# Performance work log

Measured on AMD Instinct MI355X. Metric: run time of the kernel, lower is better.

The kernel has to match this reference:

```python
import jax, jax.numpy as jnp
import numpy as np

V, D, H, L, E = 50000, 512, 512, 4, 40000


def setup_inputs() -> dict:
    key = jax.random.key(0)
    k1, k2, k3 = jax.random.split(key, 3)
    node_embeddings = jax.random.normal(k1, (V, D), dtype=jnp.float32)
    adjacency = jax.random.randint(k2, (L, E, 2), 0, V, dtype=jnp.int32)
    W = jax.random.normal(k3, (L, D, H), dtype=jnp.float32) * (1.0 / np.sqrt(D))
    return {"node_embeddings": node_embeddings, "adjacency": adjacency, "W": W}


def reference(node_embeddings, adjacency, W):
    # adjacency: [L, E, 2] with [:, :, 0] = source node, [:, :, 1] = target node
    src = adjacency[..., 0]  # [L, E]
    tgt = adjacency[..., 1]  # [L, E]
    # Gather source states per edge and apply per-edge-type linear message fn.
    # edge_source_states: [L, E, D]; messages: [L, E, H]
    messages = jnp.einsum("led,ldh->leh", node_embeddings[src], W)
    # Scatter-aggregate (sum) all messages to their target nodes.
    num_nodes = node_embeddings.shape[0]
    aggregated = jax.ops.segment_sum(
        messages.reshape(-1, messages.shape[-1]),  # [L*E, H]
        tgt.reshape(-1),
        num_segments=num_nodes,
    )  # [V, H]
    # message_activation_before_aggregation = False -> activation after aggregation
    return jax.nn.relu(aggregated)
```

## Files before the change

kernel.cpp:

```cpp
#include <hip/hip_runtime.h>
#include <hip/hip_bf16.h>

#define NV 50000
#define VP2 50176
#define ND 512
#define NH 512
#define NL 4
#define NE 40000
#define CAP 16
#define KTOT 2048
#define NKT 32
#define NWG2 392

typedef short bf16x8 __attribute__((ext_vector_type(8)));
typedef float f32x4  __attribute__((ext_vector_type(4)));

__device__ __forceinline__ unsigned short f2bf(float f) {
    unsigned int u = __float_as_uint(f);
    u += 0x7FFFu + ((u >> 16) & 1u);
    return (unsigned short)(u >> 16);
}
__device__ __forceinline__ unsigned pack_bf2(float x, float y) {
    return (unsigned)f2bf(x) | ((unsigned)f2bf(y) << 16);
}

#define GLL16(gp, lp) __builtin_amdgcn_global_load_lds( \
    (const __attribute__((address_space(1))) void*)(gp), \
    (__attribute__((address_space(3))) void*)(lp), 16, 0, 0)

__global__ void wt2_kernel(const float* __restrict__ W, unsigned short* __restrict__ Wt2) {
    int idx = blockIdx.x * 256 + threadIdx.x;
    int l = idx >> 18;
    int r = idx & 262143;
    int k = r >> 9;
    int h = r & 511;
    Wt2[((size_t)h << 11) + (l << 9) + k] = f2bf(W[idx]);
}

__global__ void place_kernel(const int* __restrict__ adj, int* __restrict__ cnt,
                             int* __restrict__ list) {
    int i = blockIdx.x * 256 + threadIdx.x;
    int2 p = ((const int2*)adj)[i];
    int l = i / NE;
    int cell = p.y * NL + l;
    int pos = atomicAdd(&cnt[cell], 1);
    if (pos < CAP) list[cell * CAP + pos] = p.x;
}

__global__ void __launch_bounds__(256)
agg_pull(const float* __restrict__ emb, const int* __restrict__ cnt,
         const int* __restrict__ list, unsigned* __restrict__ agg2) {
    const int wid  = blockIdx.x * 4 + (threadIdx.x >> 6);
    const int lane = threadIdx.x & 63;
    const int t    = wid >> 2;
    const int l    = wid & 3;
    const int cell = wid;
    const size_t dst = (size_t)t * 1024 + l * 256 + lane;

    int n = cnt[cell]; if (n > CAP) n = CAP;
    const int* lst = list + cell * CAP;

    float2 s0 = {0.f,0.f}, s1 = {0.f,0.f}, s2 = {0.f,0.f}, s3 = {0.f,0.f};
    int j = 0;
    for (; j + 2 <= n; j += 2) {
        const float2* p0 = (const float2*)(emb + (size_t)lst[j]     * ND) + lane;
        const float2* p1 = (const float2*)(emb + (size_t)lst[j + 1] * ND) + lane;
        float2 a0 = p0[0], a1 = p0[64], a2 = p0[128], a3 = p0[192];
        float2 b0 = p1[0], b1 = p1[64], b2 = p1[128], b3 = p1[192];
        s0.x += a0.x + b0.x; s0.y += a0.y + b0.y;
        s1.x += a1.x + b1.x; s1.y += a1.y + b1.y;
        s2.x += a2.x + b2.x; s2.y += a2.y + b2.y;
        s3.x += a3.x + b3.x; s3.y += a3.y + b3.y;
    }
    if (j < n) {
        const float2* p0 = (const float2*)(emb + (size_t)lst[j] * ND) + lane;
        float2 a0 = p0[0], a1 = p0[64], a2 = p0[128], a3 = p0[192];
        s0.x += a0.x; s0.y += a0.y;  s1.x += a1.x; s1.y += a1.y;
        s2.x += a2.x; s2.y += a2.y;  s3.x += a3.x; s3.y += a3.y;
    }
    agg2[dst]       = pack_bf2(s0.x, s0.y);
    agg2[dst + 64]  = pack_bf2(s1.x, s1.y);
    agg2[dst + 128] = pack_bf2(s2.x, s2.y);
    agg2[dst + 192] = pack_bf2(s3.x, s3.y);
}

__device__ __forceinline__ void stage_ht(
    int s, int t0, int n0, int wave, int lane,
    const unsigned short* __restrict__ agg2, const unsigned short* __restrict__ Wt2,
    unsigned short* sa0, unsigned short* sa1,
    unsigned short* sb0, unsigned short* sb1) {
    const int tile  = s >> 2, part = s & 3;
    const int lr8   = (part & 1) << 7;
    const int rowin = lane >> 3;
    const int slt   = (lane & 7) ^ rowin;
    const bool isA  = part < 2;
    const unsigned short* gsrc = isA ? agg2 : Wt2;
    const int gr0 = isA ? t0 : n0;
    unsigned short* ldsbase = isA ? ((tile & 1) ? sa1 : sa0)
                                  : ((tile & 1) ? sb1 : sb0);
#pragma unroll
    for (int c = 0; c < 2; ++c) {
        const int lr = lr8 + (wave * 2 + c) * 8;
        const unsigned short* src = gsrc
            + (size_t)(gr0 + lr + rowin) * KTOT + tile * 64 + slt * 8;
        GLL16(src, ldsbase + lr * 64);
    }
}

template<bool STG>
__device__ __forceinline__ void tile_step(
    int kt, int t0, int n0, int wave, int lane, int wm, int wn,
    const unsigned short* __restrict__ agg2, const unsigned short* __restrict__ Wt2,
    unsigned short* sa0, unsigned short* sa1,
    unsigned short* sb0, unsigned short* sb1,
    f32x4 (&acc)[8][4]) {
    const int laneL = lane & 15, laneH = lane >> 4;
    const int ax = laneL & 7;
    const unsigned short* pa = (kt & 1) ? sa1 : sa0;
    const unsigned short* pb = (kt & 1) ? sb1 : sb0;

    if (STG) {
        const int s1 = (kt + 1) * 4;
        stage_ht(s1 + 0, t0, n0, wave, lane, agg2, Wt2, sa0, sa1, sb0, sb1);
        stage_ht(s1 + 1, t0, n0, wave, lane, agg2, Wt2, sa0, sa1, sb0, sb1);
        stage_ht(s1 + 2, t0, n0, wave, lane, agg2, Wt2, sa0, sa1, sb0, sb1);
        stage_ht(s1 + 3, t0, n0, wave, lane, agg2, Wt2, sa0, sa1, sb0, sb1);
    }

    bf16x8 aF[4][2], bF[4][2];
#pragma unroll
    for (int ni = 0; ni < 4; ++ni)
#pragma unroll
        for (int ks = 0; ks < 2; ++ks) {
            const int row = wn * 64 + ni * 16 + laneL;
            bF[ni][ks] = *(const bf16x8*)(pb + row * 64 + (((ks * 4 + laneH) ^ ax) << 3));
        }
#pragma unroll
    for (int mi = 0; mi < 4; ++mi)
#pragma unroll
        for (int ks = 0; ks < 2; ++ks) {
            const int row = wm * 128 + mi * 16 + laneL;
            aF[mi][ks] = *(const bf16x8*)(pa + row * 64 + (((ks * 4 + laneH) ^ ax) << 3));
        }
#pragma unroll
    for (int mi = 0; mi < 4; ++mi)
#pragma unroll
        for (int ni = 0; ni < 4; ++ni)
#pragma unroll
            for (int ks = 0; ks < 2; ++ks)
                acc[mi][ni] = __builtin_amdgcn_mfma_f32_16x16x32_bf16(aF[mi][ks], bF[ni][ks], acc[mi][ni], 0, 0, 0);
#pragma unroll
    for (int mi = 0; mi < 4; ++mi)
#pragma unroll
        for (int ks = 0; ks < 2; ++ks) {
            const int row = wm * 128 + (mi + 4) * 16 + laneL;
            aF[mi][ks] = *(const bf16x8*)(pa + row * 64 + (((ks * 4 + laneH) ^ ax) << 3));
        }
#pragma unroll
    for (int mi = 0; mi < 4; ++mi)
#pragma unroll
        for (int ni = 0; ni < 4; ++ni)
#pragma unroll
            for (int ks = 0; ks < 2; ++ks)
                acc[mi + 4][ni] = __builtin_amdgcn_mfma_f32_16x16x32_bf16(aF[mi][ks], bF[ni][ks], acc[mi + 4][ni], 0, 0, 0);

    __syncthreads();
}

__global__ void __launch_bounds__(512)
gemm2p(const unsigned short* __restrict__ agg2,
       const unsigned short* __restrict__ Wt2,
       float* __restrict__ out) {
    __shared__ unsigned short s_a[2][256 * 64];
    __shared__ unsigned short s_b[2][256 * 64];

    const int orig = blockIdx.x;
    const int wgid = (orig & 7) * (NWG2 / 8) + (orig >> 3);
    const int mt = wgid >> 1, nt = wgid & 1;
    const int t0 = mt * 256, n0 = nt * 256;

    const int tid  = threadIdx.x;
    const int lane = tid & 63;
    const int wave = tid >> 6;
    const int wm   = wave >> 2;
    const int wn   = wave & 3;
    const int laneL = lane & 15, laneH = lane >> 4;

    f32x4 acc[8][4];
#pragma unroll
    for (int mi = 0; mi < 8; ++mi)
#pragma unroll
        for (int ni = 0; ni < 4; ++ni)
            acc[mi][ni] = (f32x4){0.f, 0.f, 0.f, 0.f};

    unsigned short* sa0 = &s_a[0][0]; unsigned short* sa1 = &s_a[1][0];
    unsigned short* sb0 = &s_b[0][0]; unsigned short* sb1 = &s_b[1][0];

#pragma unroll
    for (int p = 0; p < 4; ++p)
        stage_ht(p, t0, n0, wave, lane, agg2, Wt2, sa0, sa1, sb0, sb1);
    __syncthreads();

    for (int kt = 0; kt < NKT - 1; ++kt)
        tile_step<true>(kt, t0, n0, wave, lane, wm, wn, agg2, Wt2, sa0, sa1, sb0, sb1, acc);
    tile_step<false>(NKT - 1, t0, n0, wave, lane, wm, wn, agg2, Wt2, sa0, sa1, sb0, sb1, acc);

#pragma unroll
    for (int mi = 0; mi < 8; ++mi) {
#pragma unroll
        for (int i = 0; i < 4; ++i) {
            int t = t0 + wm * 128 + mi * 16 + laneH * 4 + i;
            if (t < NV) {
#pragma unroll
                for (int ni = 0; ni < 4; ++ni) {
                    int h = n0 + wn * 64 + ni * 16 + laneL;
                    out[(size_t)t * NH + h] = fmaxf(acc[mi][ni][i], 0.f);
                }
            }
        }
    }
}

__global__ void wt_legacy(const float* __restrict__ W, unsigned short* __restrict__ Wt) {
    int idx = blockIdx.x * 256 + threadIdx.x;
    int l = idx >> 18;
    int r = idx & 262143;
    int k = r >> 9;
    int h = r & 511;
    Wt[(l << 18) + (h << 9) + k] = f2bf(W[idx]);
}
__global__ void __launch_bounds__(256)
legacy_msg(const float* __restrict__ emb, const int* __restrict__ adj,
           const unsigned short* __restrict__ Wt, float* __restrict__ out) {
    __shared__ bf16x8 s_a[32 * 64];
    __shared__ int s_src[32];
    __shared__ int s_tgt[32];
    const int bx = blockIdx.x;
    const int l = bx / (NE / 32);
    const int ebase = (bx % (NE / 32)) * 32;
    const int tid = threadIdx.x, lane = tid & 63, wave = tid >> 6;
    if (tid < 32) {
        int2 p = *(const int2*)(adj + ((size_t)l * NE + ebase + tid) * 2);
        s_src[tid] = p.x; s_tgt[tid] = p.y;
    }
    __syncthreads();
    {
        const int r = tid >> 3, part = tid & 7, k0 = part * 64, rxx = r & 7;
        const float* g = emb + (size_t)s_src[r] * ND + k0;
#pragma unroll
        for (int j = 0; j < 8; ++j) {
            float4 f0 = *(const float4*)(g + j * 8);
            float4 f1 = *(const float4*)(g + j * 8 + 4);
            bf16x8 v;
            v[0]=(short)f2bf(f0.x); v[1]=(short)f2bf(f0.y);
            v[2]=(short)f2bf(f0.z); v[3]=(short)f2bf(f0.w);
            v[4]=(short)f2bf(f1.x); v[5]=(short)f2bf(f1.y);
            v[6]=(short)f2bf(f1.z); v[7]=(short)f2bf(f1.w);
            int slot = (k0 >> 3) + j;
            s_a[r * 64 + (slot ^ rxx)] = v;
        }
    }
    __syncthreads();
    const int c0 = wave * 128, laneL = lane & 15, laneH = lane >> 4, arx = laneL & 7;
    f32x4 acc[2][8];
#pragma unroll
    for (int mf = 0; mf < 2; ++mf)
#pragma unroll
        for (int nf = 0; nf < 8; ++nf) acc[mf][nf] = (f32x4){0.f,0.f,0.f,0.f};
    const bf16x8* wb = (const bf16x8*)(Wt + ((size_t)l << 18));
#pragma unroll
    for (int kc = 0; kc < 16; ++kc) {
        int slot = kc * 4 + laneH;
        bf16x8 a0 = s_a[laneL * 64 + (slot ^ arx)];
        bf16x8 a1 = s_a[(16 + laneL) * 64 + (slot ^ arx)];
#pragma unroll
        for (int nf = 0; nf < 8; ++nf) {
            bf16x8 b = wb[(c0 + nf * 16 + laneL) * 64 + slot];
            acc[0][nf] = __builtin_amdgcn_mfma_f32_16x16x32_bf16(a0, b, acc[0][nf], 0, 0, 0);
            acc[1][nf] = __builtin_amdgcn_mfma_f32_16x16x32_bf16(a1, b, acc[1][nf], 0, 0, 0);
        }
    }
#pragma unroll
    for (int mf = 0; mf < 2; ++mf)
#pragma unroll
        for (int nf = 0; nf < 8; ++nf) {
            int h = c0 + nf * 16 + laneL;
#pragma unroll
            for (int i = 0; i < 4; ++i) {
                int er = mf * 16 + laneH * 4 + i;
                atomicAdd(out + (size_t)s_tgt[er] * NH + h, acc[mf][nf][i]);
            }
        }
}
__global__ void legacy_relu(float* __restrict__ o, int n4) {
    int stride = gridDim.x * blockDim.x;
    for (int i = blockIdx.x * blockDim.x + threadIdx.x; i < n4; i += stride) {
        float4 v = ((float4*)o)[i];
        v.x = fmaxf(v.x, 0.f); v.y = fmaxf(v.y, 0.f);
        v.z = fmaxf(v.z, 0.f); v.w = fmaxf(v.w, 0.f);
        ((float4*)o)[i] = v;
    }
}

extern "C" void kernel_launch(void* const* d_in, const int* in_sizes, int n_in,
                              void* d_out, int out_size, void* d_ws, size_t ws_size,
                              hipStream_t stream) {
    const float* emb = (const float*)d_in[0];
    const int*   adj = (const int*)d_in[1];
    const float* W   = (const float*)d_in[2];
    float* out = (float*)d_out;
    char* ws = (char*)d_ws;

    unsigned short* Wt2  = (unsigned short*)ws;
    int*            cnt  = (int*)(ws + 2621440);
    int*            list = (int*)(ws + 3670016);
    unsigned short* agg2 = (unsigned short*)(ws + (16u << 20));

    const size_t need = (16u << 20) + (size_t)VP2 * KTOT * 2;

    if (ws_size >= need) {
        hipMemsetAsync(cnt, 0, (size_t)VP2 * NL * sizeof(int), stream);
        wt2_kernel<<<(NL * ND * NH) / 256, 256, 0, stream>>>(W, Wt2);
        place_kernel<<<(NL * NE) / 256, 256, 0, stream>>>(adj, cnt, list);
        agg_pull<<<(VP2 * NL) / 4, 256, 0, stream>>>(emb, cnt, list, (unsigned*)agg2);
        gemm2p<<<NWG2, 512, 0, stream>>>(agg2, Wt2, out);
    } else {
        hipMemsetAsync(d_out, 0, (size_t)out_size * sizeof(float), stream);
        wt_legacy<<<(NL * ND * NH) / 256, 256, 0, stream>>>(W, Wt2);
        legacy_msg<<<NL * (NE / 32), 256, 0, stream>>>(emb, adj, Wt2, out);
        legacy_relu<<<2048, 256, 0, stream>>>(out, out_size / 4);
    }
}
```

Baseline: 261.2 us.

## Load GEMM B fragments directly from global memory instead of staging through LDS

The GEMM kernel no longer stages the weight tile into shared memory. Each wave reads its B fragments straight from global memory (expected to hit in L2), and only the A tile is double-buffered in LDS. This halves LDS usage and the async copy traffic per tile, which could allow more workgroups per CU. The cost is exposed global-load latency on the B operand inside the MFMA loop, with no prefetch ahead of use.

```diff
diff --git a/kernel.cpp b/kernel.cpp
--- a/kernel.cpp
+++ b/kernel.cpp
@@ -84,26 +84,21 @@
     agg2[dst + 192] = pack_bf2(s3.x, s3.y);
 }
 
-__device__ __forceinline__ void stage_ht(
-    int s, int t0, int n0, int wave, int lane,
-    const unsigned short* __restrict__ agg2, const unsigned short* __restrict__ Wt2,
-    unsigned short* sa0, unsigned short* sa1,
-    unsigned short* sb0, unsigned short* sb1) {
-    const int tile  = s >> 2, part = s & 3;
-    const int lr8   = (part & 1) << 7;
+__device__ __forceinline__ void stage_a(
+    int kt, int t0, int wave, int lane,
+    const unsigned short* __restrict__ agg2,
+    unsigned short* sa0, unsigned short* sa1) {
     const int rowin = lane >> 3;
-    const int slt   = (lane & 7) ^ rowin;
-    const bool isA  = part < 2;
-    const unsigned short* gsrc = isA ? agg2 : Wt2;
-    const int gr0 = isA ? t0 : n0;
-    unsigned short* ldsbase = isA ? ((tile & 1) ? sa1 : sa0)
-                                  : ((tile & 1) ? sb1 : sb0);
-#pragma unroll
-    for (int c = 0; c < 2; ++c) {
-        const int lr = lr8 + (wave * 2 + c) * 8;
-        const unsigned short* src = gsrc
-            + (size_t)(gr0 + lr + rowin) * KTOT + tile * 64 + slt * 8;
-        GLL16(src, ldsbase + lr * 64);
+    const int slt   = lane & 7;
+    unsigned short* sa = (kt & 1) ? sa1 : sa0;
+    const int ko = kt * 64;
+#pragma unroll
+    for (int r = 0; r < 4; ++r) {
+        const int rb  = r * 64 + wave * 8;
+        const int row = rb + rowin;
+        const unsigned short* src = agg2
+            + (size_t)(t0 + row) * KTOT + ko + ((slt ^ (row & 7)) << 3);
+        GLL16(src, sa + rb * 64);
     }
 }
 
@@ -112,29 +107,24 @@
     int kt, int t0, int n0, int wave, int lane, int wm, int wn,
     const unsigned short* __restrict__ agg2, const unsigned short* __restrict__ Wt2,
     unsigned short* sa0, unsigned short* sa1,
-    unsigned short* sb0, unsigned short* sb1,
     f32x4 (&acc)[8][4]) {
     const int laneL = lane & 15, laneH = lane >> 4;
     const int ax = laneL & 7;
     const unsigned short* pa = (kt & 1) ? sa1 : sa0;
-    const unsigned short* pb = (kt & 1) ? sb1 : sb0;
-
-    if (STG) {
-        const int s1 = (kt + 1) * 4;
-        stage_ht(s1 + 0, t0, n0, wave, lane, agg2, Wt2, sa0, sa1, sb0, sb1);
-        stage_ht(s1 + 1, t0, n0, wave, lane, agg2, Wt2, sa0, sa1, sb0, sb1);
-        stage_ht(s1 + 2, t0, n0, wave, lane, agg2, Wt2, sa0, sa1, sb0, sb1);
-        stage_ht(s1 + 3, t0, n0, wave, lane, agg2, Wt2, sa0, sa1, sb0, sb1);
-    }
-
-    bf16x8 aF[4][2], bF[4][2];
+    const int ko = kt * 64;
+
+    if (STG) stage_a(kt + 1, t0, wave, lane, agg2, sa0, sa1);
+
+    bf16x8 bF[4][2];
 #pragma unroll
     for (int ni = 0; ni < 4; ++ni)
 #pragma unroll
         for (int ks = 0; ks < 2; ++ks) {
-            const int row = wn * 64 + ni * 16 + laneL;
-            bF[ni][ks] = *(const bf16x8*)(pb + row * 64 + (((ks * 4 + laneH) ^ ax) << 3));
-        }
+            const int h = n0 + wn * 64 + ni * 16 + laneL;
+            bF[ni][ks] = *(const bf16x8*)(Wt2 + (size_t)h * KTOT + ko + ks * 32 + laneH * 8);
+        }
+
+    bf16x8 aF[4][2];
 #pragma unroll
     for (int mi = 0; mi < 4; ++mi)
 #pragma unroll
@@ -168,11 +158,10 @@
 }
 
 __global__ void __launch_bounds__(512)
-gemm2p(const unsigned short* __restrict__ agg2,
-       const unsigned short* __restrict__ Wt2,
-       float* __restrict__ out) {
+gemm_bg(const unsigned short* __restrict__ agg2,
+        const unsigned short* __restrict__ Wt2,
+        float* __restrict__ out) {
     __shared__ unsigned short s_a[2][256 * 64];
-    __shared__ unsigned short s_b[2][256 * 64];
 
     const int orig = blockIdx.x;
     const int wgid = (orig & 7) * (NWG2 / 8) + (orig >> 3);
@@ -194,16 +183,13 @@
             acc[mi][ni] = (f32x4){0.f, 0.f, 0.f, 0.f};
 
     unsigned short* sa0 = &s_a[0][0]; unsigned short* sa1 = &s_a[1][0];
-    unsigned short* sb0 = &s_b[0][0]; unsigned short* sb1 = &s_b[1][0];
-
-#pragma unroll
-    for (int p = 0; p < 4; ++p)
-        stage_ht(p, t0, n0, wave, lane, agg2, Wt2, sa0, sa1, sb0, sb1);
+
+    stage_a(0, t0, wave, lane, agg2, sa0, sa1);
     __syncthreads();
 
     for (int kt = 0; kt < NKT - 1; ++kt)
-        tile_step<true>(kt, t0, n0, wave, lane, wm, wn, agg2, Wt2, sa0, sa1, sb0, sb1, acc);
-    tile_step<false>(NKT - 1, t0, n0, wave, lane, wm, wn, agg2, Wt2, sa0, sa1, sb0, sb1, acc);
+        tile_step<true>(kt, t0, n0, wave, lane, wm, wn, agg2, Wt2, sa0, sa1, acc);
+    tile_step<false>(NKT - 1, t0, n0, wave, lane, wm, wn, agg2, Wt2, sa0, sa1, acc);
 
 #pragma unroll
     for (int mi = 0; mi < 8; ++mi) {
@@ -323,7 +309,7 @@
         wt2_kernel<<<(NL * ND * NH) / 256, 256, 0, stream>>>(W, Wt2);
         place_kernel<<<(NL * NE) / 256, 256, 0, stream>>>(adj, cnt, list);
         agg_pull<<<(VP2 * NL) / 4, 256, 0, stream>>>(emb, cnt, list, (unsigned*)agg2);
-        gemm2p<<<NWG2, 512, 0, stream>>>(agg2, Wt2, out);
+        gemm_bg<<<NWG2, 512, 0, stream>>>(agg2, Wt2, out);
     } else {
         hipMemsetAsync(d_out, 0, (size_t)out_size * sizeof(float), stream);
         wt_legacy<<<(NL * ND * NH) / 256, 256, 0, stream>>>(W, Wt2);
```

Result: slower. 334.2 us (+27.9%).
